# Performance work log

Hardware: AMD Instinct MI355X
Metric: run time of the kernel (lower is better)

The kernel has to match this reference:

```python
import jax, jax.numpy as jnp
import numpy as np

N_NODES = 20000
E_RAND = 300000
IN_F, OUT_F, HEADS = 1280, 128, 4
HID = OUT_F * HEADS  # 512


def gat_conv(x, src, dst, W, attn_l, attn_r, bias, n_nodes):
    """DGL GATConv: fc (no bias) -> per-edge LeakyReLU(el_src+er_dst) ->
    segment softmax over incoming edges -> weighted scatter-sum -> +bias.
    Returns (N, HEADS, OUT_F)."""
    h = (x @ W).reshape(n_nodes, HEADS, OUT_F)            # (N,H,F)
    el = jnp.einsum('nhf,hf->nh', h, attn_l)              # (N,H)
    er = jnp.einsum('nhf,hf->nh', h, attn_r)              # (N,H)
    e = jax.nn.leaky_relu(el[src] + er[dst], 0.2)         # (E,H)
    emax = jax.ops.segment_max(e, dst, num_segments=n_nodes)
    ee = jnp.exp(e - emax[dst])                           # (E,H)
    denom = jax.ops.segment_sum(ee, dst, num_segments=n_nodes)
    alpha = ee / denom[dst]                               # (E,H)
    msg = h[src] * alpha[:, :, None]                      # (E,H,F)
    out = jax.ops.segment_sum(msg, dst, num_segments=n_nodes)
    return out + bias.reshape(HEADS, OUT_F)


def setup_inputs() -> dict:
    key = jax.random.key(0)
    ks = jax.random.split(key, 12)
    src_r = jax.random.randint(ks[0], (E_RAND,), 0, N_NODES)
    dst_r = jax.random.randint(ks[1], (E_RAND,), 0, N_NODES)
    self_loop = jnp.arange(N_NODES)
    src = jnp.concatenate([src_r, self_loop])  # self loops: contact[i][i]=1
    dst = jnp.concatenate([dst_r, self_loop])
    feature = jax.random.normal(ks[2], (N_NODES, IN_F), dtype=jnp.float32)
    s1 = 1.0 / np.sqrt(IN_F)
    s2 = 1.0 / np.sqrt(HID)
    return {
        'feature': feature,
        'W1': jax.random.normal(ks[3], (IN_F, HID), dtype=jnp.float32) * s1,
        'al1': jax.random.normal(ks[4], (HEADS, OUT_F), dtype=jnp.float32) * s2,
        'ar1': jax.random.normal(ks[5], (HEADS, OUT_F), dtype=jnp.float32) * s2,
        'b1': jnp.zeros((HID,), dtype=jnp.float32),
        'W2': jax.random.normal(ks[6], (HID, HID), dtype=jnp.float32) * s2,
        'al2': jax.random.normal(ks[7], (HEADS, OUT_F), dtype=jnp.float32) * s2,
        'ar2': jax.random.normal(ks[8], (HEADS, OUT_F), dtype=jnp.float32) * s2,
        'b2': jnp.zeros((HID,), dtype=jnp.float32),
        'Wfc': jax.random.normal(ks[9], (HID, 64), dtype=jnp.float32) * s2,
        'bfc': jnp.zeros((64,), dtype=jnp.float32),
        'src': src,
        'dst': dst,
    }


def reference(feature, W1, al1, ar1, b1, W2, al2, ar2, b2, Wfc, bfc, src, dst):
    n = feature.shape[0]
    out = gat_conv(feature, src, dst, W1, al1, ar1, b1, n)   # (N,4,128)
    out = jax.nn.elu(out).reshape(n, HID)                    # (N,512)
    out = gat_conv(out, src, dst, W2, al2, ar2, b2, n)       # (N,4,128)
    out = jax.nn.elu(out).reshape(n, HID)                    # (N,512)
    out = out @ Wfc + bfc                                    # (N,64)
    out = jax.nn.elu(out[None, :, :])                        # (1,N,64)
    return out
```

## Files before the change

kernel.cpp:

```cpp
#include <hip/hip_runtime.h>
#include <hip/hip_bf16.h>
#include <math.h>

#define HID 512
#define HEADS 4
#define OUTF 128

typedef __attribute__((ext_vector_type(8))) _Float16 f16x8_t;
typedef __attribute__((ext_vector_type(4))) _Float16 f16x4_t;
typedef __attribute__((ext_vector_type(4))) float f32x4_t;

__device__ __forceinline__ void gl_lds16(const void* g, void* l) {
    __builtin_amdgcn_global_load_lds(
        (const __attribute__((address_space(1))) void*)g,
        (__attribute__((address_space(3))) void*)l, 16, 0, 0);
}

__device__ __forceinline__ void stage_plane32(const _Float16* g, int strideE,
    int rbase, int rmax, char* plane, int tid)
{
#pragma unroll
    for (int j = 0; j < 2; ++j) {
        int gci = j * 256 + tid;
        int r = gci >> 2, c = gci & 3;
        int rg = rbase + r; if (rg > rmax) rg = rmax;
        const char* s = (const char*)(g + (size_t)rg * strideE) + ((c ^ ((r >> 1) & 3)) << 4);
        char* d = plane + (j * 256 + (tid & ~63)) * 16;
        gl_lds16(s, d);
    }
}

__global__ __launch_bounds__(256) void conv16_kernel(const float* __restrict__ in,
    _Float16* __restrict__ o, int nquad)
{
    int stride = gridDim.x * 256;
    for (int i = blockIdx.x * 256 + threadIdx.x; i < nquad; i += stride) {
        float4 v = *(const float4*)&in[(size_t)i * 4];
        f16x4_t ov;
        ov[0] = (_Float16)v.x; ov[1] = (_Float16)v.y;
        ov[2] = (_Float16)v.z; ov[3] = (_Float16)v.w;
        *(f16x4_t*)&o[(size_t)i * 4] = ov;
    }
}

__global__ __launch_bounds__(256) void prep_w(const float* __restrict__ W,
    _Float16* __restrict__ Wt, int K, int NC)
{
    __shared__ float tile[32][33];
    const int k0 = blockIdx.x * 32, n0 = blockIdx.y * 32;
    const int t = threadIdx.x;
    {
        int r = t >> 3, c4 = (t & 7) * 4;
        float4 v = *(const float4*)&W[(size_t)(k0 + r) * NC + n0 + c4];
        tile[r][c4] = v.x; tile[r][c4 + 1] = v.y;
        tile[r][c4 + 2] = v.z; tile[r][c4 + 3] = v.w;
    }
    __syncthreads();
    int n = t >> 3, kc = (t & 7) * 4;
#pragma unroll
    for (int i = 0; i < 4; ++i)
        Wt[(size_t)(n0 + n) * K + k0 + kc + i] = (_Float16)tile[kc + i][n];
}

template<int EPI, int OUT16, int ELER>
__global__ __launch_bounds__(256, 3) void gemm_f16(
    const _Float16* __restrict__ Af, const _Float16* __restrict__ Bt,
    const float* __restrict__ bias,
    const float* __restrict__ attl, const float* __restrict__ attr,
    float* __restrict__ elp, float* __restrict__ erp,
    void* __restrict__ Cout, int M, int K, int NCOL, int ldC,
    int ncolT, int nwg)
{
    __shared__ char lds[32768];
    const int tid = threadIdx.x;
    const int wave = tid >> 6, lane = tid & 63;
    const int wm = wave >> 1, wn = wave & 1;
    const int b = blockIdx.x;
    const int q = nwg >> 3, rr = nwg & 7;
    const int xcd = b & 7, ib = b >> 3;
    const int logical = (xcd < rr ? xcd * (q + 1) : rr * (q + 1) + (xcd - rr) * q) + ib;
    const int bm = (logical / ncolT) * 128, bcol = logical % ncolT;
    const int bn = bcol * 128;
    const int l15 = lane & 15, l4 = lane >> 4;
    const int swz = (l15 >> 1) & 3;

    f32x4_t acc[4][4];
#pragma unroll
    for (int i = 0; i < 4; ++i)
#pragma unroll
        for (int j = 0; j < 4; ++j) acc[i][j] = (f32x4_t){0.f, 0.f, 0.f, 0.f};

    const int nt = K >> 5;
    stage_plane32(Af, K, bm, M - 1, lds, tid);
    stage_plane32(Bt, K, bn, NCOL - 1, lds + 8192, tid);
    __syncthreads();

    for (int t = 0; t < nt; ++t) {
        char* AH = lds + (t & 1) * 16384;
        char* BH = AH + 8192;
        if (t + 1 < nt) {
            char* AHn = lds + ((t + 1) & 1) * 16384;
            stage_plane32(Af + (t + 1) * 32, K, bm, M - 1, AHn, tid);
            stage_plane32(Bt + (t + 1) * 32, K, bn, NCOL - 1, AHn + 8192, tid);
        }
        f16x8_t fa[4], fb[4];
#pragma unroll
        for (int mf = 0; mf < 4; ++mf) {
            int row = wm * 64 + mf * 16 + l15;
            fa[mf] = *(const f16x8_t*)(AH + row * 64 + ((l4 ^ swz) << 4));
        }
#pragma unroll
        for (int nf = 0; nf < 4; ++nf) {
            int rn = wn * 64 + nf * 16 + l15;
            fb[nf] = *(const f16x8_t*)(BH + rn * 64 + ((l4 ^ swz) << 4));
        }
#pragma unroll
        for (int mf = 0; mf < 4; ++mf)
#pragma unroll
            for (int nf = 0; nf < 4; ++nf)
                acc[mf][nf] = __builtin_amdgcn_mfma_f32_16x16x32_f16(fa[mf], fb[nf], acc[mf][nf], 0, 0, 0);
        __syncthreads();
    }
#pragma unroll
    for (int mf = 0; mf < 4; ++mf) {
        int rbase = bm + wm * 64 + mf * 16 + l4 * 4;
#pragma unroll
        for (int nf = 0; nf < 4; ++nf) {
            int col = bn + wn * 64 + nf * 16 + l15;
            if (col >= NCOL) continue;
#pragma unroll
            for (int r = 0; r < 4; ++r) {
                int row = rbase + r;
                if (row < M) {
                    float v = acc[mf][nf][r];
                    if (EPI) {
                        v += bias[col];
                        v = v > 0.f ? v : (expf(v) - 1.f);
                    }
                    if (OUT16) ((_Float16*)Cout)[(size_t)row * ldC + col] = (_Float16)v;
                    else       ((float*)Cout)[(size_t)row * ldC + col] = v;
                }
            }
        }
    }
    if (ELER) {
        const int head = bcol;
        float alv[4], arv[4];
#pragma unroll
        for (int nf = 0; nf < 4; ++nf) {
            int cl = wn * 64 + nf * 16 + l15;
            alv[nf] = attl[head * OUTF + cl];
            arv[nf] = attr[head * OUTF + cl];
        }
        float pel[4][4], perr[4][4];
#pragma unroll
        for (int mf = 0; mf < 4; ++mf)
#pragma unroll
            for (int r = 0; r < 4; ++r) {
                float se = 0.f, sr = 0.f;
#pragma unroll
                for (int nf = 0; nf < 4; ++nf) {
                    se = fmaf(acc[mf][nf][r], alv[nf], se);
                    sr = fmaf(acc[mf][nf][r], arv[nf], sr);
                }
                pel[mf][r] = se; perr[mf][r] = sr;
            }
#pragma unroll
        for (int off = 1; off < 16; off <<= 1)
#pragma unroll
            for (int mf = 0; mf < 4; ++mf)
#pragma unroll
                for (int r = 0; r < 4; ++r) {
                    pel[mf][r]  += __shfl_xor(pel[mf][r],  off);
                    perr[mf][r] += __shfl_xor(perr[mf][r], off);
                }
        __syncthreads();
        float* red = (float*)lds;
        if (l15 == 0) {
#pragma unroll
            for (int mf = 0; mf < 4; ++mf)
#pragma unroll
                for (int r = 0; r < 4; ++r) {
                    int rl = wm * 64 + mf * 16 + l4 * 4 + r;
                    red[rl * 2 + wn]       = pel[mf][r];
                    red[256 + rl * 2 + wn] = perr[mf][r];
                }
        }
        __syncthreads();
        if (tid < 128) {
            int row = bm + tid;
            if (row < M) {
                float es = red[tid * 2] + red[tid * 2 + 1];
                float rs = red[256 + tid * 2] + red[256 + tid * 2 + 1];
                elp[row * HEADS + head] = es;
                erp[row * HEADS + head] = rs;
            }
        }
    }
}

__global__ void hist_kernel(const int* __restrict__ dst, int* __restrict__ deg, int E)
{
    int e = blockIdx.x * 256 + threadIdx.x;
    if (e < E) atomicAdd(&deg[dst[e]], 1);
}

__global__ __launch_bounds__(256) void scan1_kernel(const int* __restrict__ deg,
    int* __restrict__ offs, int* __restrict__ bsum, int N)
{
    __shared__ int buf[256];
    int tid = threadIdx.x;
    int i = blockIdx.x * 256 + tid;
    int v = (i < N) ? deg[i] : 0;
    buf[tid] = v;
    __syncthreads();
#pragma unroll
    for (int off = 1; off < 256; off <<= 1) {
        int t = (tid >= off) ? buf[tid - off] : 0;
        __syncthreads();
        buf[tid] += t;
        __syncthreads();
    }
    if (i < N) offs[i] = buf[tid] - v;
    if (tid == 255) bsum[blockIdx.x] = buf[255];
}

__global__ void scan2_kernel(int* __restrict__ bsum, int nb)
{
    if (threadIdx.x == 0) {
        int acc = 0;
        for (int b = 0; b < nb; ++b) { int t = bsum[b]; bsum[b] = acc; acc += t; }
        bsum[nb] = acc;
    }
}

__global__ void scan3_kernel(int* __restrict__ offs, const int* __restrict__ bsum,
                             int N, int nb)
{
    int i = blockIdx.x * 256 + threadIdx.x;
    if (i < N) offs[i] += bsum[blockIdx.x];
    if (i == 0) offs[N] = bsum[nb];
}

__global__ void fill_kernel(const int* __restrict__ srcv, const int* __restrict__ dstv,
    const int* __restrict__ offs, int* __restrict__ cursor,
    int* __restrict__ psrc, int E)
{
    int e = blockIdx.x * 256 + threadIdx.x;
    if (e < E) {
        int d = dstv[e];
        int p = atomicAdd(&cursor[d], 1);
        psrc[offs[d] + p] = srcv[e];
    }
}

__global__ __launch_bounds__(64) void aggregate_kernel(const _Float16* __restrict__ h,
    const int* __restrict__ offs, const int* __restrict__ psrc,
    const float* __restrict__ el, const float* __restrict__ er,
    const float* __restrict__ bias, _Float16* __restrict__ xo, int N)
{
    __shared__ int ssm[64];
    __shared__ float wsm[4][64];
    int n = blockIdx.x;
    int lane = threadIdx.x;
    int c = lane * 8;
    int head = lane >> 4;
    float4 erv = *(const float4*)&er[n * HEADS];
    float acc[8];
#pragma unroll
    for (int k = 0; k < 8; ++k) acc[k] = 0.f;
    float ws = 0.f;
    int beg = offs[n], end = offs[n + 1];
    for (int base = beg; base < end; base += 64) {
        int cnt = min(64, end - base);
        if (lane < cnt) {
            int s = psrc[base + lane];
            float4 lv = *(const float4*)&el[s * HEADS];
            float x;
            x = lv.x + erv.x; x = x > 0.f ? x : 0.2f * x; wsm[0][lane] = expf(x);
            x = lv.y + erv.y; x = x > 0.f ? x : 0.2f * x; wsm[1][lane] = expf(x);
            x = lv.z + erv.z; x = x > 0.f ? x : 0.2f * x; wsm[2][lane] = expf(x);
            x = lv.w + erv.w; x = x > 0.f ? x : 0.2f * x; wsm[3][lane] = expf(x);
            ssm[lane] = s;
        }
        __syncthreads();
        int j = 0;
        for (; j + 4 <= cnt; j += 4) {
            int s0 = ssm[j], s1 = ssm[j + 1], s2 = ssm[j + 2], s3 = ssm[j + 3];
            float w0 = wsm[head][j],     w1 = wsm[head][j + 1];
            float w2 = wsm[head][j + 2], w3 = wsm[head][j + 3];
            f16x8_t v0 = *(const f16x8_t*)&h[(size_t)s0 * HID + c];
            f16x8_t v1 = *(const f16x8_t*)&h[(size_t)s1 * HID + c];
            f16x8_t v2 = *(const f16x8_t*)&h[(size_t)s2 * HID + c];
            f16x8_t v3 = *(const f16x8_t*)&h[(size_t)s3 * HID + c];
#pragma unroll
            for (int k = 0; k < 8; ++k) {
                acc[k] = fmaf(w0, (float)v0[k], acc[k]);
                acc[k] = fmaf(w1, (float)v1[k], acc[k]);
                acc[k] = fmaf(w2, (float)v2[k], acc[k]);
                acc[k] = fmaf(w3, (float)v3[k], acc[k]);
            }
            ws += w0 + w1 + w2 + w3;
        }
        for (; j < cnt; ++j) {
            int s0 = ssm[j];
            float w0 = wsm[head][j];
            f16x8_t v0 = *(const f16x8_t*)&h[(size_t)s0 * HID + c];
#pragma unroll
            for (int k = 0; k < 8; ++k) acc[k] = fmaf(w0, (float)v0[k], acc[k]);
            ws += w0;
        }
        __syncthreads();
    }
    float inv = 1.f / ws;
    float4 b0 = *(const float4*)&bias[c];
    float4 b1 = *(const float4*)&bias[c + 4];
    float bb[8] = {b0.x, b0.y, b0.z, b0.w, b1.x, b1.y, b1.z, b1.w};
    f16x8_t ov;
#pragma unroll
    for (int k = 0; k < 8; ++k) {
        float r = acc[k] * inv + bb[k];
        r = r > 0.f ? r : (expf(r) - 1.f);
        ov[k] = (_Float16)r;
    }
    *(f16x8_t*)&xo[(size_t)n * HID + c] = ov;
}

extern "C" void kernel_launch(void* const* d_in, const int* in_sizes, int n_in,
                              void* d_out, int out_size, void* d_ws, size_t ws_size,
                              hipStream_t stream)
{
    const float* feature = (const float*)d_in[0];
    const float* W1  = (const float*)d_in[1];
    const float* al1 = (const float*)d_in[2];
    const float* ar1 = (const float*)d_in[3];
    const float* b1  = (const float*)d_in[4];
    const float* W2  = (const float*)d_in[5];
    const float* al2 = (const float*)d_in[6];
    const float* ar2 = (const float*)d_in[7];
    const float* b2  = (const float*)d_in[8];
    const float* Wfc = (const float*)d_in[9];
    const float* bfc = (const float*)d_in[10];
    const int* src = (const int*)d_in[11];
    const int* dst = (const int*)d_in[12];
    const int N = in_sizes[0] / 1280;
    const int E = in_sizes[11];
    const int nb = (N + 255) / 256;
    float* out = (float*)d_out;

    char* ws = (char*)d_ws;
    size_t off = 0;
    auto alloc = [&](size_t bytes) {
        void* p = ws + off;
        off += (bytes + 255) & ~(size_t)255;
        return p;
    };
    int* deg    = (int*)alloc((size_t)N * 4);
    int* cursor = (int*)alloc((size_t)N * 4);
    int* offs   = (int*)alloc((size_t)(N + 1) * 4);
    int* bsum   = (int*)alloc((size_t)(nb + 1) * 4);
    float* el   = (float*)alloc((size_t)N * HEADS * 4);
    float* er   = (float*)alloc((size_t)N * HEADS * 4);
    int* psrc   = (int*)alloc((size_t)E * 4);
    _Float16* featf = (_Float16*)alloc((size_t)N * 1280 * 2);
    _Float16* hbuf  = (_Float16*)alloc((size_t)N * HID * 2);
    _Float16* xh    = (_Float16*)alloc((size_t)N * HID * 2);
    _Float16* W1t   = (_Float16*)alloc((size_t)HID * 1280 * 2);
    _Float16* W2t   = (_Float16*)alloc((size_t)HID * HID * 2);
    _Float16* Wft   = (_Float16*)alloc((size_t)64 * HID * 2);

    hipMemsetAsync(deg, 0, (size_t)N * 4, stream);
    hipMemsetAsync(cursor, 0, (size_t)N * 4, stream);
    hist_kernel<<<(E + 255) / 256, 256, 0, stream>>>(dst, deg, E);
    scan1_kernel<<<nb, 256, 0, stream>>>(deg, offs, bsum, N);
    scan2_kernel<<<1, 64, 0, stream>>>(bsum, nb);
    scan3_kernel<<<nb, 256, 0, stream>>>(offs, bsum, N, nb);
    fill_kernel<<<(E + 255) / 256, 256, 0, stream>>>(src, dst, offs, cursor, psrc, E);

    conv16_kernel<<<2048, 256, 0, stream>>>(feature, featf, N * 1280 / 4);
    prep_w<<<dim3(1280 / 32, HID / 32), 256, 0, stream>>>(W1, W1t, 1280, HID);
    prep_w<<<dim3(HID / 32, HID / 32), 256, 0, stream>>>(W2, W2t, HID, HID);
    prep_w<<<dim3(HID / 32, 64 / 32), 256, 0, stream>>>(Wfc, Wft, HID, 64);

    const int nrowT = (N + 127) / 128;
    const int nwgG = nrowT * (HID / 128);
    const int nwgF = nrowT;

    gemm_f16<0, 1, 1><<<nwgG, 256, 0, stream>>>(featf, W1t, nullptr,
                                                al1, ar1, el, er,
                                                hbuf, N, 1280, HID, HID,
                                                HID / 128, nwgG);
    aggregate_kernel<<<N, 64, 0, stream>>>(hbuf, offs, psrc, el, er, b1, xh, N);

    gemm_f16<0, 1, 1><<<nwgG, 256, 0, stream>>>(xh, W2t, nullptr,
                                                al2, ar2, el, er,
                                                hbuf, N, HID, HID, HID,
                                                HID / 128, nwgG);
    aggregate_kernel<<<N, 64, 0, stream>>>(hbuf, offs, psrc, el, er, b2, xh, N);

    gemm_f16<1, 0, 0><<<nwgF, 256, 0, stream>>>(xh, Wft, bfc,
                                                nullptr, nullptr, nullptr, nullptr,
                                                out, N, HID, 64, 64,
                                                1, nwgF);
}
```

Before: 262.0 us.

## Pack four nodes per aggregate block and broadcast edge weights via wave shuffles

The aggregation kernel now handles four destination nodes per 256-thread block, one wavefront per node, instead of one node per 64-thread block. Edge source indices and softmax weights are computed per chunk of 32 edges and broadcast with __shfl rather than staged through LDS with __syncthreads. Each half-wave computes the exp for two heads, which cuts barrier and LDS traffic and the launch of many tiny blocks. In exchange each lane issues more shuffle and select operations per edge.

```diff
diff --git a/kernel.cpp b/kernel.cpp
--- a/kernel.cpp
+++ b/kernel.cpp
@@ -254,41 +254,52 @@
     }
 }
 
-__global__ __launch_bounds__(64) void aggregate_kernel(const _Float16* __restrict__ h,
+__global__ __launch_bounds__(256) void aggregate_kernel(const _Float16* __restrict__ h,
     const int* __restrict__ offs, const int* __restrict__ psrc,
     const float* __restrict__ el, const float* __restrict__ er,
     const float* __restrict__ bias, _Float16* __restrict__ xo, int N)
 {
-    __shared__ int ssm[64];
-    __shared__ float wsm[4][64];
-    int n = blockIdx.x;
-    int lane = threadIdx.x;
-    int c = lane * 8;
-    int head = lane >> 4;
-    float4 erv = *(const float4*)&er[n * HEADS];
+    const int n = blockIdx.x * 4 + (threadIdx.x >> 6);
+    if (n >= N) return;
+    const int lane = threadIdx.x & 63;
+    const int c = lane * 8;
+    const int head = lane >> 4;
+    const int hp = lane >> 5;
+    const int e31 = lane & 31;
+    const int sbase = (head >> 1) << 5;
+    const int hsel = head & 1;
+
+    const float2 er2 = *(const float2*)&er[n * HEADS + hp * 2];
+
     float acc[8];
 #pragma unroll
     for (int k = 0; k < 8; ++k) acc[k] = 0.f;
     float ws = 0.f;
-    int beg = offs[n], end = offs[n + 1];
-    for (int base = beg; base < end; base += 64) {
-        int cnt = min(64, end - base);
-        if (lane < cnt) {
-            int s = psrc[base + lane];
-            float4 lv = *(const float4*)&el[s * HEADS];
-            float x;
-            x = lv.x + erv.x; x = x > 0.f ? x : 0.2f * x; wsm[0][lane] = expf(x);
-            x = lv.y + erv.y; x = x > 0.f ? x : 0.2f * x; wsm[1][lane] = expf(x);
-            x = lv.z + erv.z; x = x > 0.f ? x : 0.2f * x; wsm[2][lane] = expf(x);
-            x = lv.w + erv.w; x = x > 0.f ? x : 0.2f * x; wsm[3][lane] = expf(x);
-            ssm[lane] = s;
-        }
-        __syncthreads();
+
+    const int beg = offs[n], end = offs[n + 1];
+    for (int base = beg; base < end; base += 32) {
+        const int cnt = min(32, end - base);
+        int idx = base + e31;
+        if (e31 >= cnt) idx = beg;
+        const int s = psrc[idx];
+        const float2 lv = *(const float2*)&el[s * HEADS + hp * 2];
+        float x0 = lv.x + er2.x; x0 = x0 > 0.f ? x0 : 0.2f * x0;
+        float x1 = lv.y + er2.y; x1 = x1 > 0.f ? x1 : 0.2f * x1;
+        const float wa = expf(x0);
+        const float wb = expf(x1);
+
         int j = 0;
         for (; j + 4 <= cnt; j += 4) {
-            int s0 = ssm[j], s1 = ssm[j + 1], s2 = ssm[j + 2], s3 = ssm[j + 3];
-            float w0 = wsm[head][j],     w1 = wsm[head][j + 1];
-            float w2 = wsm[head][j + 2], w3 = wsm[head][j + 3];
+            int s0 = __shfl(s, j);     int s1 = __shfl(s, j + 1);
+            int s2 = __shfl(s, j + 2); int s3 = __shfl(s, j + 3);
+            float a0 = __shfl(wa, sbase + j),     b0 = __shfl(wb, sbase + j);
+            float a1 = __shfl(wa, sbase + j + 1), b1 = __shfl(wb, sbase + j + 1);
+            float a2 = __shfl(wa, sbase + j + 2), b2 = __shfl(wb, sbase + j + 2);
+            float a3 = __shfl(wa, sbase + j + 3), b3 = __shfl(wb, sbase + j + 3);
+            float w0 = hsel ? b0 : a0;
+            float w1 = hsel ? b1 : a1;
+            float w2 = hsel ? b2 : a2;
+            float w3 = hsel ? b3 : a3;
             f16x8_t v0 = *(const f16x8_t*)&h[(size_t)s0 * HID + c];
             f16x8_t v1 = *(const f16x8_t*)&h[(size_t)s1 * HID + c];
             f16x8_t v2 = *(const f16x8_t*)&h[(size_t)s2 * HID + c];
@@ -303,19 +314,19 @@
             ws += w0 + w1 + w2 + w3;
         }
         for (; j < cnt; ++j) {
-            int s0 = ssm[j];
-            float w0 = wsm[head][j];
+            int s0 = __shfl(s, j);
+            float a0 = __shfl(wa, sbase + j), b0 = __shfl(wb, sbase + j);
+            float w0 = hsel ? b0 : a0;
             f16x8_t v0 = *(const f16x8_t*)&h[(size_t)s0 * HID + c];
 #pragma unroll
             for (int k = 0; k < 8; ++k) acc[k] = fmaf(w0, (float)v0[k], acc[k]);
             ws += w0;
         }
-        __syncthreads();
     }
     float inv = 1.f / ws;
-    float4 b0 = *(const float4*)&bias[c];
-    float4 b1 = *(const float4*)&bias[c + 4];
-    float bb[8] = {b0.x, b0.y, b0.z, b0.w, b1.x, b1.y, b1.z, b1.w};
+    float4 b0v = *(const float4*)&bias[c];
+    float4 b1v = *(const float4*)&bias[c + 4];
+    float bb[8] = {b0v.x, b0v.y, b0v.z, b0v.w, b1v.x, b1v.y, b1v.z, b1v.w};
     f16x8_t ov;
 #pragma unroll
     for (int k = 0; k < 8; ++k) {
@@ -385,18 +396,19 @@
     const int nrowT = (N + 127) / 128;
     const int nwgG = nrowT * (HID / 128);
     const int nwgF = nrowT;
+    const int aggB = (N + 3) / 4;
 
     gemm_f16<0, 1, 1><<<nwgG, 256, 0, stream>>>(featf, W1t, nullptr,
                                                 al1, ar1, el, er,
                                                 hbuf, N, 1280, HID, HID,
                                                 HID / 128, nwgG);
-    aggregate_kernel<<<N, 64, 0, stream>>>(hbuf, offs, psrc, el, er, b1, xh, N);
+    aggregate_kernel<<<aggB, 256, 0, stream>>>(hbuf, offs, psrc, el, er, b1, xh, N);
 
     gemm_f16<0, 1, 1><<<nwgG, 256, 0, stream>>>(xh, W2t, nullptr,
                                                 al2, ar2, el, er,
                                                 hbuf, N, HID, HID, HID,
                                                 HID / 128, nwgG);
-    aggregate_kernel<<<N, 64, 0, stream>>>(hbuf, offs, psrc, el, er, b2, xh, N);
+    aggregate_kernel<<<aggB, 256, 0, stream>>>(hbuf, offs, psrc, el, er, b2, xh, N);
 
     gemm_f16<1, 0, 0><<<nwgF, 256, 0, stream>>>(xh, Wft, bfc,
                                                 nullptr, nullptr, nullptr, nullptr,
```

After: 260.3 us. No clear change (-0.6%).
